# Performance work log

Measured on AMD Instinct MI355X. Metric: run time of the kernel, lower is better.

Reference implementation:

```python
import jax, jax.numpy as jnp
import numpy as np

N_NODES = 100000
THETA = jnp.asarray([0.2, -0.4, 0.3, -0.15, 0.05], dtype=jnp.float32)


def setup_inputs() -> dict:
    key = jax.random.key(0)
    k1, k2, k3, k4 = jax.random.split(key, 4)
    n_edges = 1600000
    feat = jax.random.normal(k1, (N_NODES, 32), dtype=jnp.float32)
    src = jax.random.randint(k2, (n_edges,), 0, N_NODES, dtype=jnp.int32)
    dst = jax.random.randint(k3, (n_edges,), 0, N_NODES, dtype=jnp.int32)
    mask = jax.random.uniform(k4, (n_edges,), dtype=jnp.float32)
    return {"feat": feat, "src": src, "dst": dst, "mask": mask}


def reference(feat, src, dst, mask):
    # degree = sum of edge mask into destination nodes (copy_e + sum)
    deg = jax.ops.segment_sum(mask, dst, num_segments=N_NODES)
    # D^{-1/2} with clamp(min=1)
    d_invsqrt = jnp.power(jnp.maximum(deg, 1.0), -0.5)[:, None]  # [N,1]

    h = THETA[0] * feat
    for k in range(1, THETA.shape[0]):
        # unnormalized Laplacian step: feat - D^{-1/2} A D^{-1/2} feat
        scaled = feat * d_invsqrt                      # [N,d]
        msg = scaled[src] * mask[:, None]              # [E,d] gather + edge scale
        agg = jax.ops.segment_sum(msg, dst, num_segments=N_NODES)  # [N,d]
        feat = feat - agg * d_invsqrt
        h = h + THETA[k] * feat
    return h
```

## Files before the change

kernel.cpp:

```cpp
#include <hip/hip_runtime.h>
#include <hip/hip_fp16.h>


#define FDIM 32
#define DLO_BITS 8
#define BKT_NODES 256
#define NBLK 1024
#define MAXBKT 512


__global__ __launch_bounds__(256) void p1_kernel(const int* __restrict__ dst,
                                                 int* __restrict__ cntT,
                                                 int nbkt, int S, int E) {
    __shared__ int lh[MAXBKT];
    int b = blockIdx.x;
    for (int t = threadIdx.x; t < MAXBKT; t += 256) lh[t] = 0;
    __syncthreads();
    int e0 = b * S;
    int e1 = e0 + S < E ? e0 + S : E;
    for (int e = e0 + threadIdx.x; e < e1; e += 256)
        atomicAdd(&lh[dst[e] >> DLO_BITS], 1);
    __syncthreads();
    for (int t = threadIdx.x; t < nbkt; t += 256) cntT[t * NBLK + b] = lh[t];
}

__global__ void scanA_kernel(const int* __restrict__ cntT, int* __restrict__ obase,
                             int* __restrict__ bsums, int M2) {
    int tid = threadIdx.x;
    int gid = blockIdx.x * 256 + tid;
    int v = (gid < M2) ? cntT[gid] : 0;
    int lane = tid & 63, wv = tid >> 6;
    int x = v;
#pragma unroll
    for (int o = 1; o < 64; o <<= 1) {
        int y = __shfl_up(x, o);
        if (lane >= o) x += y;
    }
    __shared__ int ws[4];
    if (lane == 63) ws[wv] = x;
    __syncthreads();
    int add = 0;
    for (int i = 0; i < wv; ++i) add += ws[i];
    x += add;
    if (gid < M2) obase[gid] = x - v;
    if (tid == 255) bsums[blockIdx.x] = x;
}

__global__ void scan2_kernel(int* __restrict__ bsums, int nb) {
    __shared__ int ws[8];
    __shared__ int carry;
    if (threadIdx.x == 0) carry = 0;
    __syncthreads();
    for (int base = 0; base < nb; base += 512) {
        int i = base + threadIdx.x;
        int v = (i < nb) ? bsums[i] : 0;
        int lane = threadIdx.x & 63, wv = threadIdx.x >> 6;
        int x = v;
#pragma unroll
        for (int o = 1; o < 64; o <<= 1) {
            int y = __shfl_up(x, o);
            if (lane >= o) x += y;
        }
        if (lane == 63) ws[wv] = x;
        __syncthreads();
        int add = 0;
        for (int j = 0; j < wv; ++j) add += ws[j];
        x += add;
        int c = carry;
        if (i < nb) bsums[i] = x - v + c;
        __syncthreads();
        if (threadIdx.x == 511) carry = c + x;
        __syncthreads();
    }
}

__global__ void scanC_kernel(int* __restrict__ obase, const int* __restrict__ bsums, int M2) {
    int gid = blockIdx.x * 256 + threadIdx.x;
    if (gid < M2) obase[gid] += bsums[blockIdx.x];
}

__global__ __launch_bounds__(256) void p3_kernel(const int* __restrict__ src,
                                                 const int* __restrict__ dst,
                                                 const float* __restrict__ mask,
                                                 const int* __restrict__ obase,
                                                 int2* __restrict__ esp,
                                                 int S, int E) {
    __shared__ int lh[MAXBKT];
    int b = blockIdx.x;
    for (int t = threadIdx.x; t < MAXBKT; t += 256) lh[t] = 0;
    __syncthreads();
    int e0 = b * S;
    int e1 = e0 + S < E ? e0 + S : E;
    for (int e = e0 + threadIdx.x; e < e1; e += 256) {
        int d = dst[e];
        int g = d >> DLO_BITS;
        int r = atomicAdd(&lh[g], 1);
        int pos = obase[g * NBLK + b] + r;
        int2 v;
        v.x = src[e] | ((d & (BKT_NODES - 1)) << 17);
        v.y = __float_as_int(mask[e]);
        esp[pos] = v;
    }
}

__global__ __launch_bounds__(512) void p4_kernel(const int2* __restrict__ esp,
                                                 const int* __restrict__ obase,
                                                 int* __restrict__ esI,
                                                 int* __restrict__ row_ptr,
                                                 float* __restrict__ dinv,
                                                 const float4* __restrict__ feat,
                                                 uint2* __restrict__ m0,
                                                 int nbkt, int N, int E) {
    __shared__ int lcnt[BKT_NODES];
    __shared__ int lofs[BKT_NODES];
    __shared__ float ldeg[BKT_NODES];
    __shared__ int ws[8];
    int g = blockIdx.x;
    int tid = threadIdx.x;
    if (tid < BKT_NODES) { lcnt[tid] = 0; ldeg[tid] = 0.0f; }
    __syncthreads();
    int segbase = obase[g * NBLK];
    int segend = (g + 1 < nbkt) ? obase[(g + 1) * NBLK] : E;
    for (int i = segbase + tid; i < segend; i += 512) {
        int2 v = esp[i];
        int dlo = v.x >> 17;
        atomicAdd(&lcnt[dlo], 1);
        atomicAdd(&ldeg[dlo], __int_as_float(v.y));
    }
    __syncthreads();
    int v = (tid < BKT_NODES) ? lcnt[tid] : 0;
    int lane = tid & 63, wv = tid >> 6;
    int x = v;
#pragma unroll
    for (int o = 1; o < 64; o <<= 1) {
        int y = __shfl_up(x, o);
        if (lane >= o) x += y;
    }
    if (lane == 63) ws[wv] = x;
    __syncthreads();
    int add = 0;
    for (int i = 0; i < wv; ++i) add += ws[i];
    x += add;
    int excl = x - v;
    if (tid < BKT_NODES) {
        lofs[tid] = excl;
        int node = g * BKT_NODES + tid;
        if (node < N) {
            row_ptr[node] = segbase + excl;
            float d = ldeg[tid];
            d = d > 1.0f ? d : 1.0f;
            float di = 1.0f / sqrtf(d);
            dinv[node] = di;
            ldeg[tid] = di;
        }
    }
    if (g == 0 && tid == 0) row_ptr[N] = E;
    __syncthreads();
    if (tid < BKT_NODES) lcnt[tid] = 0;
    __syncthreads();
    for (int i = segbase + tid; i < segend; i += 512) {
        int2 v2 = esp[i];
        int dlo = v2.x >> 17;
        int r = atomicAdd(&lcnt[dlo], 1);
        float mk = __int_as_float(v2.y);
        int wq = (int)(mk * 32768.0f + 0.5f);
        if (wq > 32767) wq = 32767;
        esI[segbase + lofs[dlo] + r] = (v2.x & 0x1FFFF) | (wq << 17);
    }
    int base_node = g * BKT_NODES;
    for (int t = tid; t < BKT_NODES * 8; t += 512) {
        int nl = t >> 3;
        int n2 = base_node + nl;
        if (n2 >= N) break;
        float di = ldeg[nl];
        float4 f = feat[(size_t)n2 * 8 + (t & 7)];
        __half2 a = __float22half2_rn(make_float2(f.x * di, f.y * di));
        __half2 b = __float22half2_rn(make_float2(f.z * di, f.w * di));
        uint2 m;
        m.x = *(unsigned*)&a;
        m.y = *(unsigned*)&b;
        m0[(size_t)n2 * 8 + (t & 7)] = m;
    }
}

template <int MODE>
__global__ __launch_bounds__(256) void aggregate_kernel(
    const float4* __restrict__ fown, float4* __restrict__ fwr,
    const uint2* __restrict__ gin, uint2* __restrict__ gout,
    float4* __restrict__ out,
    const int* __restrict__ row_ptr, const int* __restrict__ es,
    const float* __restrict__ dinv, float theta, float theta0, int N) {
    int wave = (blockIdx.x * blockDim.x + threadIdx.x) >> 6;
    int lane = threadIdx.x & 63;
    int node = wave * 4 + (lane >> 4);
    if (node >= N) return;
    int l16 = lane & 15;
    int c = l16 & 7;
    int q = l16 >> 3;
    int b = row_ptr[node];
    int e = row_ptr[node + 1];
    float ax = 0.f, ay = 0.f, az = 0.f, aw = 0.f;
    float bx = 0.f, by = 0.f, bz = 0.f, bw = 0.f;
    int i = b + q;
    for (; i + 2 < e; i += 4) {
        int e0 = es[i];
        int e1 = es[i + 2];
        float w0 = (float)((unsigned)e0 >> 17) * (1.0f / 32768.0f);
        float w1 = (float)((unsigned)e1 >> 17) * (1.0f / 32768.0f);
        uint2 r0 = gin[(size_t)(e0 & 0x1FFFF) * 8 + c];
        uint2 r1 = gin[(size_t)(e1 & 0x1FFFF) * 8 + c];
        float2 p0 = __half22float2(*(const __half2*)&r0.x);
        float2 p1 = __half22float2(*(const __half2*)&r0.y);
        float2 p2 = __half22float2(*(const __half2*)&r1.x);
        float2 p3 = __half22float2(*(const __half2*)&r1.y);
        ax += w0 * p0.x; ay += w0 * p0.y; az += w0 * p1.x; aw += w0 * p1.y;
        bx += w1 * p2.x; by += w1 * p2.y; bz += w1 * p3.x; bw += w1 * p3.y;
    }
    if (i < e) {
        int e0 = es[i];
        float w0 = (float)((unsigned)e0 >> 17) * (1.0f / 32768.0f);
        uint2 r0 = gin[(size_t)(e0 & 0x1FFFF) * 8 + c];
        float2 p0 = __half22float2(*(const __half2*)&r0.x);
        float2 p1 = __half22float2(*(const __half2*)&r0.y);
        ax += w0 * p0.x; ay += w0 * p0.y; az += w0 * p1.x; aw += w0 * p1.y;
    }
    ax += bx; ay += by; az += bz; aw += bw;
    ax += __shfl_xor(ax, 8);
    ay += __shfl_xor(ay, 8);
    az += __shfl_xor(az, 8);
    aw += __shfl_xor(aw, 8);
    float4 fav = fown[(size_t)node * 8 + c];
    float di = dinv[node];
    float fx = fav.x - ax * di;
    float fy = fav.y - ay * di;
    float fz = fav.z - az * di;
    float fw = fav.w - aw * di;
    if (MODE != 2) {
        if (q == 0) {
            float4 t; t.x = fx; t.y = fy; t.z = fz; t.w = fw;
            fwr[(size_t)node * 8 + c] = t;
            __half2 a = __float22half2_rn(make_float2(fx * di, fy * di));
            __half2 bb = __float22half2_rn(make_float2(fz * di, fw * di));
            uint2 m;
            m.x = *(unsigned*)&a;
            m.y = *(unsigned*)&bb;
            gout[(size_t)node * 8 + c] = m;
        } else {
            float4 o;
            if (MODE == 1) {
                o.x = theta0 * fav.x + theta * fx;
                o.y = theta0 * fav.y + theta * fy;
                o.z = theta0 * fav.z + theta * fz;
                o.w = theta0 * fav.w + theta * fw;
            } else {
                o = out[(size_t)node * 8 + c];
                o.x += theta * fx; o.y += theta * fy;
                o.z += theta * fz; o.w += theta * fw;
            }
            out[(size_t)node * 8 + c] = o;
        }
    } else {
        if (q == 1) {
            float4 o = out[(size_t)node * 8 + c];
            o.x += theta * fx; o.y += theta * fy;
            o.z += theta * fz; o.w += theta * fw;
            out[(size_t)node * 8 + c] = o;
        }
    }
}


__global__ void fb_deg_kernel(const int* __restrict__ dst, const float* __restrict__ mask,
                              float* __restrict__ deg, int E) {
    int e = blockIdx.x * blockDim.x + threadIdx.x;
    if (e < E) atomicAdd(&deg[dst[e]], mask[e]);
}

__global__ void fb_dinv_kernel(float* __restrict__ deg, int N) {
    int i = blockIdx.x * blockDim.x + threadIdx.x;
    if (i < N) {
        float d = deg[i];
        d = d > 1.0f ? d : 1.0f;
        deg[i] = 1.0f / sqrtf(d);
    }
}

__global__ void fb_init_kernel(const float4* __restrict__ feat, float4* __restrict__ fbuf,
                               float4* __restrict__ out, int n4) {
    int i = blockIdx.x * blockDim.x + threadIdx.x;
    if (i < n4) {
        float4 f = feat[i];
        fbuf[i] = f;
        float4 o;
        o.x = 0.2f * f.x; o.y = 0.2f * f.y; o.z = 0.2f * f.z; o.w = 0.2f * f.w;
        out[i] = o;
    }
}

__global__ void fb_scatter_kernel(const float4* __restrict__ fbuf, const float* __restrict__ dinv,
                                  const int* __restrict__ src, const int* __restrict__ dst,
                                  const float* __restrict__ mask, float* __restrict__ agg, int E) {
    int t = blockIdx.x * blockDim.x + threadIdx.x;
    int e = t >> 3;
    if (e >= E) return;
    int c4 = t & 7;
    int s = src[e];
    int d = dst[e];
    float w = mask[e] * dinv[s];
    float4 f = fbuf[s * 8 + c4];
    float* ap = agg + (size_t)d * FDIM + c4 * 4;
    atomicAdd(ap + 0, f.x * w);
    atomicAdd(ap + 1, f.y * w);
    atomicAdd(ap + 2, f.z * w);
    atomicAdd(ap + 3, f.w * w);
}

__global__ void fb_update_kernel(float4* __restrict__ fbuf, float4* __restrict__ agg,
                                 const float* __restrict__ dinv, float4* __restrict__ out,
                                 float theta, int n4) {
    int t = blockIdx.x * blockDim.x + threadIdx.x;
    if (t >= n4) return;
    int node = t >> 3;
    float di = dinv[node];
    float4 a = agg[t];
    float4 z; z.x = 0.f; z.y = 0.f; z.z = 0.f; z.w = 0.f;
    agg[t] = z;
    float4 f = fbuf[t];
    f.x -= a.x * di; f.y -= a.y * di; f.z -= a.z * di; f.w -= a.w * di;
    fbuf[t] = f;
    float4 o = out[t];
    o.x += theta * f.x; o.y += theta * f.y; o.z += theta * f.z; o.w += theta * f.w;
    out[t] = o;
}


static inline size_t align_up(size_t x) { return (x + 63) & ~(size_t)63; }

extern "C" void kernel_launch(void* const* d_in, const int* in_sizes, int n_in,
                              void* d_out, int out_size, void* d_ws, size_t ws_size,
                              hipStream_t stream) {
    const float* feat = (const float*)d_in[0];
    const int* src = (const int*)d_in[1];
    const int* dst = (const int*)d_in[2];
    const float* mask = (const float*)d_in[3];
    float* out = (float*)d_out;

    const int N = in_sizes[0] / FDIM;
    const int E = in_sizes[1];
    const float thetas[5] = {0.2f, -0.4f, 0.3f, -0.15f, 0.05f};
    const int B = 256;

    const int nbkt = (N + BKT_NODES - 1) / BKT_NODES;
    const int M2 = nbkt * NBLK;
    const int S = (E + NBLK - 1) / NBLK;
    const int nbM2 = (M2 + B - 1) / B;

    size_t o_dinv = 0;
    size_t o_rp   = align_up(o_dinv + N);
    size_t o_esI  = align_up(o_rp + N + 1);
    size_t o_m0   = align_up(o_esI + (size_t)E);
    size_t o_m1   = align_up(o_m0 + (size_t)N * 16);
    size_t o_big  = align_up(o_m1 + (size_t)N * 16);
    size_t o_esp  = o_big;
    size_t o_cntT = align_up(o_esp + 2 * (size_t)E);
    size_t o_ob   = align_up(o_cntT + (size_t)M2);
    size_t o_bs   = align_up(o_ob + (size_t)M2);
    size_t build_end = o_bs + 4096;
    size_t o_f    = o_big;
    size_t agg_end = o_f + (size_t)N * FDIM;
    size_t need = (build_end > agg_end ? build_end : agg_end) * 4;

    float* wsf = (float*)d_ws;
    int* wsi = (int*)d_ws;

    int nbE = (E + B - 1) / B;
    int nbN = (N + B - 1) / B;

    if (ws_size >= need && N <= (1 << 17) && nbkt <= MAXBKT && nbM2 <= 4096) {
        float* dinv = wsf + o_dinv;
        int* row_ptr = wsi + o_rp;
        int* esI = wsi + o_esI;
        uint2* m0 = (uint2*)(wsi + o_m0);
        uint2* m1 = (uint2*)(wsi + o_m1);
        int2* esp = (int2*)(wsi + o_esp);
        int* cntT = wsi + o_cntT;
        int* obase = wsi + o_ob;
        int* bsums = wsi + o_bs;
        float4* f = (float4*)(wsf + o_f);

        p1_kernel<<<NBLK, B, 0, stream>>>(dst, cntT, nbkt, S, E);
        scanA_kernel<<<nbM2, B, 0, stream>>>(cntT, obase, bsums, M2);
        scan2_kernel<<<1, 512, 0, stream>>>(bsums, nbM2);
        scanC_kernel<<<nbM2, B, 0, stream>>>(obase, bsums, M2);
        p3_kernel<<<NBLK, B, 0, stream>>>(src, dst, mask, obase, esp, S, E);
        p4_kernel<<<nbkt, 512, 0, stream>>>(esp, obase, esI, row_ptr, dinv,
                                            (const float4*)feat, m0, nbkt, N, E);

        int aggWaves = (N + 3) / 4;
        int agg_blocks = (aggWaves * 64 + B - 1) / B;
        aggregate_kernel<1><<<agg_blocks, B, 0, stream>>>((const float4*)feat, f, m0, m1,
                                                          (float4*)out, row_ptr, esI, dinv,
                                                          thetas[1], thetas[0], N);
        aggregate_kernel<0><<<agg_blocks, B, 0, stream>>>(f, f, m1, m0, (float4*)out,
                                                          row_ptr, esI, dinv, thetas[2], 0.f, N);
        aggregate_kernel<0><<<agg_blocks, B, 0, stream>>>(f, f, m0, m1, (float4*)out,
                                                          row_ptr, esI, dinv, thetas[3], 0.f, N);
        aggregate_kernel<2><<<agg_blocks, B, 0, stream>>>(f, f, m1, m0, (float4*)out,
                                                          row_ptr, esI, dinv, thetas[4], 0.f, N);
    } else {
        float* deg = wsf;
        float* agg = deg + align_up(N);
        float* fbuf = agg + (size_t)N * FDIM;

        hipMemsetAsync(d_ws, 0, (align_up(N) + (size_t)N * FDIM) * 4, stream);
        fb_deg_kernel<<<nbE, B, 0, stream>>>(dst, mask, deg, E);
        fb_dinv_kernel<<<nbN, B, 0, stream>>>(deg, N);

        int n4 = N * (FDIM / 4);
        fb_init_kernel<<<(n4 + B - 1) / B, B, 0, stream>>>((const float4*)feat, (float4*)fbuf,
                                                           (float4*)out, n4);
        long long sc_threads = (long long)E * 8;
        int sc_blocks = (int)((sc_threads + B - 1) / B);
        for (int k = 1; k < 5; ++k) {
            fb_scatter_kernel<<<sc_blocks, B, 0, stream>>>((const float4*)fbuf, deg, src, dst,
                                                           mask, agg, E);
            fb_update_kernel<<<(n4 + B - 1) / B, B, 0, stream>>>((float4*)fbuf, (float4*)agg,
                                                                 deg, (float4*)out, thetas[k], n4);
        }
    }
}
```

Baseline: 194.3 us.

## Replace global count-scan-scatter edge bucketing with per-block local sort and run reads

The five-kernel edge bucketing pipeline (histogram, three-level scan, scatter) becomes one kernel. Each block stages a fixed-size edge chunk in shared memory, counts it and sorts it locally by destination bucket, writing per-block offsets into a transposed table. A small kernel sums those offsets per bucket to get global segment bases. p4 then walks each block's run for its bucket instead of one contiguous segment. This cuts launches and avoids reading src/dst/mask twice, at the cost of short, serial, poorly coalesced run reads in p4 and a larger workspace, since the feature buffer no longer aliases the edge buffer.

Result: no change. 193.3 us (-0.5%).

```diff
diff --git a/kernel.cpp b/kernel.cpp
--- a/kernel.cpp
+++ b/kernel.cpp
@@ -5,30 +5,37 @@
 #define FDIM 32
 #define DLO_BITS 8
 #define BKT_NODES 256
-#define NBLK 1024
+#define S_FIX 1536
 #define MAXBKT 512
 
 
-__global__ __launch_bounds__(256) void p1_kernel(const int* __restrict__ dst,
-                                                 int* __restrict__ cntT,
-                                                 int nbkt, int S, int E) {
+__global__ __launch_bounds__(512) void p3_kernel(const int* __restrict__ src,
+                                                 const int* __restrict__ dst,
+                                                 const float* __restrict__ mask,
+                                                 int* __restrict__ lofsT,
+                                                 int2* __restrict__ esp,
+                                                 int NBLKp, int nbkt, int E) {
+    __shared__ int sdst[S_FIX];
+    __shared__ int ssrc[S_FIX];
+    __shared__ float smask[S_FIX];
     __shared__ int lh[MAXBKT];
+    __shared__ int ws[8];
     int b = blockIdx.x;
-    for (int t = threadIdx.x; t < MAXBKT; t += 256) lh[t] = 0;
-    __syncthreads();
-    int e0 = b * S;
-    int e1 = e0 + S < E ? e0 + S : E;
-    for (int e = e0 + threadIdx.x; e < e1; e += 256)
-        atomicAdd(&lh[dst[e] >> DLO_BITS], 1);
-    __syncthreads();
-    for (int t = threadIdx.x; t < nbkt; t += 256) cntT[t * NBLK + b] = lh[t];
-}
-
-__global__ void scanA_kernel(const int* __restrict__ cntT, int* __restrict__ obase,
-                             int* __restrict__ bsums, int M2) {
     int tid = threadIdx.x;
-    int gid = blockIdx.x * 256 + tid;
-    int v = (gid < M2) ? cntT[gid] : 0;
+    int e0 = b * S_FIX;
+    int n = E - e0;
+    if (n > S_FIX) n = S_FIX;
+    if (n < 0) n = 0;
+    for (int t = tid; t < n; t += 512) {
+        sdst[t] = dst[e0 + t];
+        ssrc[t] = src[e0 + t];
+        smask[t] = mask[e0 + t];
+    }
+    lh[tid] = 0;
+    __syncthreads();
+    for (int t = tid; t < n; t += 512) atomicAdd(&lh[sdst[t] >> DLO_BITS], 1);
+    __syncthreads();
+    int v = lh[tid];
     int lane = tid & 63, wv = tid >> 6;
     int x = v;
 #pragma unroll
@@ -36,81 +43,50 @@
         int y = __shfl_up(x, o);
         if (lane >= o) x += y;
     }
-    __shared__ int ws[4];
     if (lane == 63) ws[wv] = x;
     __syncthreads();
     int add = 0;
     for (int i = 0; i < wv; ++i) add += ws[i];
     x += add;
-    if (gid < M2) obase[gid] = x - v;
-    if (tid == 255) bsums[blockIdx.x] = x;
-}
-
-__global__ void scan2_kernel(int* __restrict__ bsums, int nb) {
-    __shared__ int ws[8];
-    __shared__ int carry;
-    if (threadIdx.x == 0) carry = 0;
-    __syncthreads();
-    for (int base = 0; base < nb; base += 512) {
-        int i = base + threadIdx.x;
-        int v = (i < nb) ? bsums[i] : 0;
-        int lane = threadIdx.x & 63, wv = threadIdx.x >> 6;
-        int x = v;
+    int excl = x - v;
+    lh[tid] = excl;
+    if (tid < nbkt) lofsT[(size_t)tid * NBLKp + b] = excl;
+    if (tid == 0) lofsT[(size_t)nbkt * NBLKp + b] = n;
+    __syncthreads();
+    for (int t = tid; t < n; t += 512) {
+        int d = sdst[t];
+        int g = d >> DLO_BITS;
+        int pos = e0 + atomicAdd(&lh[g], 1);
+        int2 vv;
+        vv.x = ssrc[t] | ((d & (BKT_NODES - 1)) << 17);
+        vv.y = __float_as_int(smask[t]);
+        esp[pos] = vv;
+    }
+}
+
+__global__ void scanR_kernel(const int* __restrict__ lofsT, int* __restrict__ R, int NBLKp) {
+    int g = blockIdx.x;
+    int tid = threadIdx.x;
+    int s = 0;
+    for (int t = tid; t < NBLKp; t += 256) s += lofsT[(size_t)g * NBLKp + t];
 #pragma unroll
-        for (int o = 1; o < 64; o <<= 1) {
-            int y = __shfl_up(x, o);
-            if (lane >= o) x += y;
-        }
-        if (lane == 63) ws[wv] = x;
-        __syncthreads();
-        int add = 0;
-        for (int j = 0; j < wv; ++j) add += ws[j];
-        x += add;
-        int c = carry;
-        if (i < nb) bsums[i] = x - v + c;
-        __syncthreads();
-        if (threadIdx.x == 511) carry = c + x;
-        __syncthreads();
-    }
-}
-
-__global__ void scanC_kernel(int* __restrict__ obase, const int* __restrict__ bsums, int M2) {
-    int gid = blockIdx.x * 256 + threadIdx.x;
-    if (gid < M2) obase[gid] += bsums[blockIdx.x];
-}
-
-__global__ __launch_bounds__(256) void p3_kernel(const int* __restrict__ src,
-                                                 const int* __restrict__ dst,
-                                                 const float* __restrict__ mask,
-                                                 const int* __restrict__ obase,
-                                                 int2* __restrict__ esp,
-                                                 int S, int E) {
-    __shared__ int lh[MAXBKT];
-    int b = blockIdx.x;
-    for (int t = threadIdx.x; t < MAXBKT; t += 256) lh[t] = 0;
-    __syncthreads();
-    int e0 = b * S;
-    int e1 = e0 + S < E ? e0 + S : E;
-    for (int e = e0 + threadIdx.x; e < e1; e += 256) {
-        int d = dst[e];
-        int g = d >> DLO_BITS;
-        int r = atomicAdd(&lh[g], 1);
-        int pos = obase[g * NBLK + b] + r;
-        int2 v;
-        v.x = src[e] | ((d & (BKT_NODES - 1)) << 17);
-        v.y = __float_as_int(mask[e]);
-        esp[pos] = v;
-    }
+    for (int o = 1; o < 64; o <<= 1) s += __shfl_xor(s, o);
+    __shared__ int wsum[4];
+    int lane = tid & 63, wv = tid >> 6;
+    if (lane == 0) wsum[wv] = s;
+    __syncthreads();
+    if (tid == 0) R[g] = wsum[0] + wsum[1] + wsum[2] + wsum[3];
 }
 
 __global__ __launch_bounds__(512) void p4_kernel(const int2* __restrict__ esp,
-                                                 const int* __restrict__ obase,
+                                                 const int* __restrict__ lofsT,
+                                                 const int* __restrict__ R,
                                                  int* __restrict__ esI,
                                                  int* __restrict__ row_ptr,
                                                  float* __restrict__ dinv,
                                                  const float4* __restrict__ feat,
                                                  uint2* __restrict__ m0,
-                                                 int nbkt, int N, int E) {
+                                                 int NBLKp, int nbkt, int N, int E) {
     __shared__ int lcnt[BKT_NODES];
     __shared__ int lofs[BKT_NODES];
     __shared__ float ldeg[BKT_NODES];
@@ -119,13 +95,17 @@
     int tid = threadIdx.x;
     if (tid < BKT_NODES) { lcnt[tid] = 0; ldeg[tid] = 0.0f; }
     __syncthreads();
-    int segbase = obase[g * NBLK];
-    int segend = (g + 1 < nbkt) ? obase[(g + 1) * NBLK] : E;
-    for (int i = segbase + tid; i < segend; i += 512) {
-        int2 v = esp[i];
-        int dlo = v.x >> 17;
-        atomicAdd(&lcnt[dlo], 1);
-        atomicAdd(&ldeg[dlo], __int_as_float(v.y));
+    int segbase = R[g];
+    for (int b = tid; b < NBLKp; b += 512) {
+        int st = lofsT[(size_t)g * NBLKp + b];
+        int en = lofsT[(size_t)(g + 1) * NBLKp + b];
+        int base = b * S_FIX;
+        for (int i = st; i < en; ++i) {
+            int2 v = esp[base + i];
+            int dlo = v.x >> 17;
+            atomicAdd(&lcnt[dlo], 1);
+            atomicAdd(&ldeg[dlo], __int_as_float(v.y));
+        }
     }
     __syncthreads();
     int v = (tid < BKT_NODES) ? lcnt[tid] : 0;
@@ -158,14 +138,19 @@
     __syncthreads();
     if (tid < BKT_NODES) lcnt[tid] = 0;
     __syncthreads();
-    for (int i = segbase + tid; i < segend; i += 512) {
-        int2 v2 = esp[i];
-        int dlo = v2.x >> 17;
-        int r = atomicAdd(&lcnt[dlo], 1);
-        float mk = __int_as_float(v2.y);
-        int wq = (int)(mk * 32768.0f + 0.5f);
-        if (wq > 32767) wq = 32767;
-        esI[segbase + lofs[dlo] + r] = (v2.x & 0x1FFFF) | (wq << 17);
+    for (int b = tid; b < NBLKp; b += 512) {
+        int st = lofsT[(size_t)g * NBLKp + b];
+        int en = lofsT[(size_t)(g + 1) * NBLKp + b];
+        int base = b * S_FIX;
+        for (int i = st; i < en; ++i) {
+            int2 v2 = esp[base + i];
+            int dlo = v2.x >> 17;
+            int r = atomicAdd(&lcnt[dlo], 1);
+            float mk = __int_as_float(v2.y);
+            int wq = (int)(mk * 32768.0f + 0.5f);
+            if (wq > 32767) wq = 32767;
+            esI[segbase + lofs[dlo] + r] = (v2.x & 0x1FFFF) | (wq << 17);
+        }
     }
     int base_node = g * BKT_NODES;
     for (int t = tid; t < BKT_NODES * 8; t += 512) {
@@ -175,10 +160,10 @@
         float di = ldeg[nl];
         float4 f = feat[(size_t)n2 * 8 + (t & 7)];
         __half2 a = __float22half2_rn(make_float2(f.x * di, f.y * di));
-        __half2 b = __float22half2_rn(make_float2(f.z * di, f.w * di));
+        __half2 bb = __float22half2_rn(make_float2(f.z * di, f.w * di));
         uint2 m;
         m.x = *(unsigned*)&a;
-        m.y = *(unsigned*)&b;
+        m.y = *(unsigned*)&bb;
         m0[(size_t)n2 * 8 + (t & 7)] = m;
     }
 }
@@ -351,24 +336,18 @@
     const int B = 256;
 
     const int nbkt = (N + BKT_NODES - 1) / BKT_NODES;
-    const int M2 = nbkt * NBLK;
-    const int S = (E + NBLK - 1) / NBLK;
-    const int nbM2 = (M2 + B - 1) / B;
+    const int NBLKp = (E + S_FIX - 1) / S_FIX;
 
     size_t o_dinv = 0;
-    size_t o_rp   = align_up(o_dinv + N);
-    size_t o_esI  = align_up(o_rp + N + 1);
-    size_t o_m0   = align_up(o_esI + (size_t)E);
-    size_t o_m1   = align_up(o_m0 + (size_t)N * 16);
-    size_t o_big  = align_up(o_m1 + (size_t)N * 16);
-    size_t o_esp  = o_big;
-    size_t o_cntT = align_up(o_esp + 2 * (size_t)E);
-    size_t o_ob   = align_up(o_cntT + (size_t)M2);
-    size_t o_bs   = align_up(o_ob + (size_t)M2);
-    size_t build_end = o_bs + 4096;
-    size_t o_f    = o_big;
-    size_t agg_end = o_f + (size_t)N * FDIM;
-    size_t need = (build_end > agg_end ? build_end : agg_end) * 4;
+    size_t o_rp    = align_up(o_dinv + N);
+    size_t o_esI   = align_up(o_rp + N + 1);
+    size_t o_m0    = align_up(o_esI + (size_t)E);
+    size_t o_m1    = align_up(o_m0 + (size_t)N * 16);
+    size_t o_esp   = align_up(o_m1 + (size_t)N * 16);
+    size_t o_lofsT = align_up(o_esp + 2 * (size_t)E);
+    size_t o_R     = align_up(o_lofsT + (size_t)(nbkt + 1) * NBLKp);
+    size_t o_f     = align_up(o_R + nbkt + 1);
+    size_t need = (o_f + (size_t)N * FDIM) * 4;
 
     float* wsf = (float*)d_ws;
     int* wsi = (int*)d_ws;
@@ -376,25 +355,21 @@
     int nbE = (E + B - 1) / B;
     int nbN = (N + B - 1) / B;
 
-    if (ws_size >= need && N <= (1 << 17) && nbkt <= MAXBKT && nbM2 <= 4096) {
+    if (ws_size >= need && N <= (1 << 17) && nbkt <= MAXBKT) {
         float* dinv = wsf + o_dinv;
         int* row_ptr = wsi + o_rp;
         int* esI = wsi + o_esI;
         uint2* m0 = (uint2*)(wsi + o_m0);
         uint2* m1 = (uint2*)(wsi + o_m1);
         int2* esp = (int2*)(wsi + o_esp);
-        int* cntT = wsi + o_cntT;
-        int* obase = wsi + o_ob;
-        int* bsums = wsi + o_bs;
+        int* lofsT = wsi + o_lofsT;
+        int* R = wsi + o_R;
         float4* f = (float4*)(wsf + o_f);
 
-        p1_kernel<<<NBLK, B, 0, stream>>>(dst, cntT, nbkt, S, E);
-        scanA_kernel<<<nbM2, B, 0, stream>>>(cntT, obase, bsums, M2);
-        scan2_kernel<<<1, 512, 0, stream>>>(bsums, nbM2);
-        scanC_kernel<<<nbM2, B, 0, stream>>>(obase, bsums, M2);
-        p3_kernel<<<NBLK, B, 0, stream>>>(src, dst, mask, obase, esp, S, E);
-        p4_kernel<<<nbkt, 512, 0, stream>>>(esp, obase, esI, row_ptr, dinv,
-                                            (const float4*)feat, m0, nbkt, N, E);
+        p3_kernel<<<NBLKp, 512, 0, stream>>>(src, dst, mask, lofsT, esp, NBLKp, nbkt, E);
+        scanR_kernel<<<nbkt + 1, 256, 0, stream>>>(lofsT, R, NBLKp);
+        p4_kernel<<<nbkt, 512, 0, stream>>>(esp, lofsT, R, esI, row_ptr, dinv,
+                                            (const float4*)feat, m0, NBLKp, nbkt, N, E);
 
         int aggWaves = (N + 3) / 4;
         int agg_blocks = (aggWaves * 64 + B - 1) / B;
```
